# Kernel optimization log

Measured on AMD Instinct MI355X. Metric: run time of the kernel, lower is better.

The kernel has to match this reference:

```python
import math
import jax, jax.numpy as jnp
import numpy as np

LAMDA = 0.5
ALPHA = 0.1
N_NODES = 100000
N_EDGES = 1600000
NFEAT = 512
NHID = 128
NCLASS = 40
NLAYER = 4


def setup_inputs() -> dict:
    key = jax.random.key(0)
    ks = jax.random.split(key, 9)
    x = jax.random.normal(ks[0], (N_NODES, NFEAT), dtype=jnp.float32)
    rows = jnp.sort(jax.random.randint(ks[1], (N_EDGES,), 0, N_NODES, dtype=jnp.int32))
    cols = jax.random.randint(ks[2], (N_EDGES,), 0, N_NODES, dtype=jnp.int32)
    # positive edge weights (stand-in for symmetric-normalized adjacency values)
    vals = jax.random.uniform(ks[3], (N_EDGES,), dtype=jnp.float32) * 0.1
    stdv_hid = 1.0 / math.sqrt(NHID)
    fc1_w = jax.random.normal(ks[4], (NFEAT, NHID), dtype=jnp.float32) * 0.02
    fc1_b = jnp.zeros((NHID,), dtype=jnp.float32)
    conv_w = jax.random.uniform(ks[5], (NLAYER, NHID, NHID), dtype=jnp.float32,
                                minval=-stdv_hid, maxval=stdv_hid)
    fc2_w = jax.random.normal(ks[6], (NHID, NCLASS), dtype=jnp.float32) * 0.02
    fc2_b = jnp.zeros((NCLASS,), dtype=jnp.float32)
    return {"x": x, "rows": rows, "cols": cols, "vals": vals,
            "fc1_w": fc1_w, "fc1_b": fc1_b, "conv_w": conv_w,
            "fc2_w": fc2_w, "fc2_b": fc2_b}


def reference(x, rows, cols, vals, fc1_w, fc1_b, conv_w, fc2_w, fc2_b):
    n = x.shape[0]
    # input projection + relu (dropout is identity in eval mode)
    h = jax.nn.relu(x @ fc1_w + fc1_b)  # [N, nhid]
    h0 = h
    for i in range(conv_w.shape[0]):
        theta = math.log(LAMDA / (i + 1) + 1.0)
        # sparse spmm: hi = A @ h  via gather + segment-sum scatter
        hi = jax.ops.segment_sum(vals[:, None] * h[cols], rows, num_segments=n)
        support = (1.0 - ALPHA) * hi + ALPHA * h0  # initial-residual mix
        h = jax.nn.relu(theta * (support @ conv_w[i]) + (1.0 - theta) * support)
    logits = h @ fc2_w + fc2_b  # [N, nclass]
    return (jax.nn.log_softmax(logits, axis=1), h, jnp.concatenate([h, logits], axis=1))
```

## Files before the change

kernel.cpp:

```cpp
#include <hip/hip_runtime.h>
#include <math.h>

#define N_NODES 100000
#define NFEAT 512
#define NHID 128
#define NCLASS 40

typedef unsigned int uint;
typedef unsigned short ushort;
typedef short bf16x8 __attribute__((ext_vector_type(8)));
typedef float f32x4 __attribute__((ext_vector_type(4)));

__device__ inline ushort bf16s(float a) {
    uint u = __float_as_uint(a);
    return (ushort)((u + 0x7fffu + ((u >> 16) & 1u)) >> 16);
}
__device__ inline uint bf16pack(float a, float b) {
    return (uint)bf16s(a) | ((uint)bf16s(b) << 16);
}
__device__ inline float bf16tof(ushort u) { return __uint_as_float(((uint)u) << 16); }
__device__ inline float bflo(uint u) { return __uint_as_float(u << 16); }
__device__ inline float bfhi(uint u) { return __uint_as_float(u & 0xffff0000u); }

__global__ void prep_weights(const float* __restrict__ fc1_w, const float* __restrict__ conv_w,
                             ushort* __restrict__ wT1, ushort* __restrict__ wTc) {
    int idx = blockIdx.x * 256 + threadIdx.x;
    {   int n = idx >> 9, k = idx & 511;
        wT1[idx] = bf16s(fc1_w[k * NHID + n]); }
    {   int L = idx >> 14, rem = idx & 16383;
        int n = rem >> 7, k = rem & 127;
        wTc[idx] = bf16s(conv_w[L * 16384 + k * NHID + n]); }
}

__global__ void rowptr_kernel(const int* __restrict__ rows, int* __restrict__ rowptr, int nE) {
    int i = blockIdx.x * blockDim.x + threadIdx.x;
    if (i > N_NODES) return;
    int lo = 0, hi = nE;
    while (lo < hi) { int mid = (lo + hi) >> 1; if (rows[mid] < i) lo = mid + 1; else hi = mid; }
    rowptr[i] = lo;
}

__global__ void __launch_bounds__(256) fc1_mfma(const float* __restrict__ x,
                                                const uint* __restrict__ wT1,
                                                const float* __restrict__ bias,
                                                ushort* __restrict__ h0b) {
    __shared__ ushort As[32][72];
    __shared__ ushort Bs[128][72];
    const int tid = threadIdx.x;
    const int lane = tid & 63;
    const int wave = tid >> 6;
    const int wr = wave >> 1, wc = wave & 1;
    const int r0 = blockIdx.x * 32;

    f32x4 acc[4] = {};

    for (int ks = 0; ks < NFEAT; ks += 64) {
        {   int row = tid >> 3, kq = tid & 7;
            const float* xp = x + (size_t)(r0 + row) * NFEAT + ks + kq * 8;
            float4 v0 = *reinterpret_cast<const float4*>(xp);
            float4 v1 = *reinterpret_cast<const float4*>(xp + 4);
            uint4 pk;
            pk.x = bf16pack(v0.x, v0.y); pk.y = bf16pack(v0.z, v0.w);
            pk.z = bf16pack(v1.x, v1.y); pk.w = bf16pack(v1.z, v1.w);
            *reinterpret_cast<uint4*>(&As[row][kq * 8]) = pk;
        }
        #pragma unroll
        for (int p = 0; p < 4; ++p) {
            int idx = tid + p * 256;
            int n = idx >> 3, q = idx & 7;
            uint4 w4 = *reinterpret_cast<const uint4*>(wT1 + n * 256 + (ks >> 1) + q * 4);
            *reinterpret_cast<uint4*>(&Bs[n][q * 8]) = w4;
        }
        __syncthreads();
        #pragma unroll
        for (int ks2 = 0; ks2 < 64; ks2 += 32) {
            bf16x8 a = *reinterpret_cast<const bf16x8*>(&As[wr * 16 + (lane & 15)][ks2 + (lane >> 4) * 8]);
            #pragma unroll
            for (int j = 0; j < 4; ++j) {
                bf16x8 b = *reinterpret_cast<const bf16x8*>(&Bs[wc * 64 + j * 16 + (lane & 15)][ks2 + (lane >> 4) * 8]);
                acc[j] = __builtin_amdgcn_mfma_f32_16x16x32_bf16(a, b, acc[j], 0, 0, 0);
            }
        }
        __syncthreads();
    }

    const int cb = wc * 64 + (lane & 15);
    const int rb = r0 + wr * 16 + ((lane >> 4) << 2);
    #pragma unroll
    for (int j = 0; j < 4; ++j) {
        int col = cb + j * 16;
        float bj = bias[col];
        #pragma unroll
        for (int i = 0; i < 4; ++i) {
            float v = fmaxf(acc[j][i] + bj, 0.f);
            h0b[(size_t)(rb + i) * NHID + col] = bf16s(v);
        }
    }
}

__global__ void __launch_bounds__(256) layer_mfma(const uint* __restrict__ sb,
                                                  const uint* __restrict__ wTc,
                                                  float theta,
                                                  ushort* __restrict__ hb,
                                                  float* __restrict__ fout) {
    __shared__ ushort As[64][136];
    __shared__ ushort Bs[128][136];
    const int tid = threadIdx.x;
    const int lane = tid & 63;
    const int wave = tid >> 6;
    const int wr = wave >> 1, wc = wave & 1;
    const int r0 = blockIdx.x * 64;

    #pragma unroll
    for (int p = 0; p < 4; ++p) {
        int idx = tid + p * 256;
        int row = idx >> 4, kq = idx & 15;
        uint4 v = *reinterpret_cast<const uint4*>(sb + (size_t)(r0 + row) * 64 + kq * 4);
        *reinterpret_cast<uint4*>(&As[row][kq * 8]) = v;
    }
    #pragma unroll
    for (int p = 0; p < 8; ++p) {
        int idx = tid + p * 256;
        int n = idx >> 4, kq = idx & 15;
        uint4 v = *reinterpret_cast<const uint4*>(wTc + n * 64 + kq * 4);
        *reinterpret_cast<uint4*>(&Bs[n][kq * 8]) = v;
    }
    __syncthreads();

    f32x4 acc[2][4] = {};
    #pragma unroll
    for (int ks = 0; ks < NHID; ks += 32) {
        #pragma unroll
        for (int mr = 0; mr < 2; ++mr) {
            bf16x8 a = *reinterpret_cast<const bf16x8*>(&As[wr * 32 + mr * 16 + (lane & 15)][ks + (lane >> 4) * 8]);
            #pragma unroll
            for (int j = 0; j < 4; ++j) {
                bf16x8 b = *reinterpret_cast<const bf16x8*>(&Bs[wc * 64 + j * 16 + (lane & 15)][ks + (lane >> 4) * 8]);
                acc[mr][j] = __builtin_amdgcn_mfma_f32_16x16x32_bf16(a, b, acc[mr][j], 0, 0, 0);
            }
        }
    }

    const float om = 1.f - theta;
    const int cb = wc * 64 + (lane & 15);
    #pragma unroll
    for (int mr = 0; mr < 2; ++mr) {
        const int rloc = wr * 32 + mr * 16 + ((lane >> 4) << 2);
        #pragma unroll
        for (int j = 0; j < 4; ++j) {
            int col = cb + j * 16;
            #pragma unroll
            for (int i = 0; i < 4; ++i) {
                int gr = r0 + rloc + i;
                if (gr < N_NODES) {
                    float s = bf16tof(As[rloc + i][col]);
                    float v = fmaxf(fmaf(theta, acc[mr][j][i], om * s), 0.f);
                    if (fout) fout[(size_t)gr * NHID + col] = v;
                    else      hb[(size_t)gr * NHID + col] = bf16s(v);
                }
            }
        }
    }
}

__global__ void spmm_kernel(const uint4* __restrict__ hb4, const uint4* __restrict__ h0b4,
                            const int* __restrict__ rowptr, const int* __restrict__ cols,
                            const float* __restrict__ vals, uint4* __restrict__ sb4) {
    const int node = blockIdx.x * 4 + (threadIdx.x >> 6);
    const int lane = threadIdx.x & 63;
    const int q = lane >> 4;
    const int l = lane & 15;

    const int e0 = rowptr[node], e1 = rowptr[node + 1];

    float a0 = 0.f, a1 = 0.f, a2 = 0.f, a3 = 0.f;
    float a4 = 0.f, a5 = 0.f, a6 = 0.f, a7 = 0.f;
    for (int base = e0; base < e1; base += 64) {
        int m = e1 - base; if (m > 64) m = 64;
        int c = 0; float v = 0.f;
        if (lane < m) { c = cols[base + lane]; v = vals[base + lane]; }
        const int nt = (m + 3) >> 2;
        #pragma unroll 8
        for (int t = 0; t < nt; ++t) {
            int j = 4 * t + q;
            int jc = (j < m) ? j : 0;
            int   cj = __shfl(c, jc);
            float vj = __shfl(v, jc);
            if (j >= m) vj = 0.f;
            uint4 hv = hb4[(size_t)cj * 16 + l];
            a0 = fmaf(vj, bflo(hv.x), a0);
            a1 = fmaf(vj, bfhi(hv.x), a1);
            a2 = fmaf(vj, bflo(hv.y), a2);
            a3 = fmaf(vj, bfhi(hv.y), a3);
            a4 = fmaf(vj, bflo(hv.z), a4);
            a5 = fmaf(vj, bfhi(hv.z), a5);
            a6 = fmaf(vj, bflo(hv.w), a6);
            a7 = fmaf(vj, bfhi(hv.w), a7);
        }
    }
    a0 += __shfl_xor(a0, 16); a1 += __shfl_xor(a1, 16);
    a2 += __shfl_xor(a2, 16); a3 += __shfl_xor(a3, 16);
    a4 += __shfl_xor(a4, 16); a5 += __shfl_xor(a5, 16);
    a6 += __shfl_xor(a6, 16); a7 += __shfl_xor(a7, 16);
    a0 += __shfl_xor(a0, 32); a1 += __shfl_xor(a1, 32);
    a2 += __shfl_xor(a2, 32); a3 += __shfl_xor(a3, 32);
    a4 += __shfl_xor(a4, 32); a5 += __shfl_xor(a5, 32);
    a6 += __shfl_xor(a6, 32); a7 += __shfl_xor(a7, 32);

    if (q == 0) {
        uint4 h0v = h0b4[(size_t)node * 16 + l];
        uint4 o;
        o.x = bf16pack(0.9f * a0 + 0.1f * bflo(h0v.x), 0.9f * a1 + 0.1f * bfhi(h0v.x));
        o.y = bf16pack(0.9f * a2 + 0.1f * bflo(h0v.y), 0.9f * a3 + 0.1f * bfhi(h0v.y));
        o.z = bf16pack(0.9f * a4 + 0.1f * bflo(h0v.z), 0.9f * a5 + 0.1f * bfhi(h0v.z));
        o.w = bf16pack(0.9f * a6 + 0.1f * bflo(h0v.w), 0.9f * a7 + 0.1f * bfhi(h0v.w));
        sb4[(size_t)node * 16 + l] = o;
    }
}

__global__ void final_kernel(const float* __restrict__ h, const float* __restrict__ w,
                             const float* __restrict__ b, float* __restrict__ out0,
                             float* __restrict__ out2) {
    __shared__ float hs[4][128];
    const int s = threadIdx.x >> 6;
    const int lane = threadIdx.x & 63;
    const int node = blockIdx.x * 4 + s;

    float h_lo = h[node * NHID + lane];
    float h_hi = h[node * NHID + 64 + lane];
    hs[s][lane] = h_lo;
    hs[s][64 + lane] = h_hi;
    __syncthreads();

    float logit = 0.f;
    if (lane < NCLASS) {
        logit = b[lane];
        #pragma unroll 8
        for (int k = 0; k < NHID; ++k)
            logit = fmaf(hs[s][k], w[k * NCLASS + lane], logit);
    }

    float mv = (lane < NCLASS) ? logit : -1e30f;
    #pragma unroll
    for (int m = 32; m; m >>= 1) mv = fmaxf(mv, __shfl_xor(mv, m));
    float ev = (lane < NCLASS) ? __expf(logit - mv) : 0.f;
    float sum = ev;
    #pragma unroll
    for (int m = 32; m; m >>= 1) sum += __shfl_xor(sum, m);
    float lse = mv + __logf(sum);

    if (lane < NCLASS) {
        out0[node * NCLASS + lane] = logit - lse;
        out2[node * 168 + 128 + lane] = logit;
    }
    out2[node * 168 + lane] = h_lo;
    out2[node * 168 + 64 + lane] = h_hi;
}

extern "C" void kernel_launch(void* const* d_in, const int* in_sizes, int n_in,
                              void* d_out, int out_size, void* d_ws, size_t ws_size,
                              hipStream_t stream) {
    const float* x      = (const float*)d_in[0];
    const int*   rows   = (const int*)  d_in[1];
    const int*   cols   = (const int*)  d_in[2];
    const float* vals   = (const float*)d_in[3];
    const float* fc1_w  = (const float*)d_in[4];
    const float* fc1_b  = (const float*)d_in[5];
    const float* conv_w = (const float*)d_in[6];
    const float* fc2_w  = (const float*)d_in[7];
    const float* fc2_b  = (const float*)d_in[8];
    float* out = (float*)d_out;

    const int nE = in_sizes[1];
    const size_t NH = (size_t)N_NODES * NHID;
    const size_t PAD = 64 * NHID;

    char* p = (char*)d_ws;
    int*    rowptr = (int*)p;          p += 400128;
    ushort* h0b    = (ushort*)p;       p += NH * 2;
    ushort* hb     = (ushort*)p;       p += (NH + PAD) * 2;
    ushort* sb     = (ushort*)p;       p += (NH + PAD) * 2;
    ushort* wT1    = (ushort*)p;       p += 65536 * 2;
    ushort* wTc    = (ushort*)p;       p += 65536 * 2;

    float* out0 = out;
    float* out1 = out + (size_t)N_NODES * NCLASS;
    float* out2 = out1 + NH;

    prep_weights<<<256, 256, 0, stream>>>(fc1_w, conv_w, wT1, wTc);
    rowptr_kernel<<<(N_NODES + 1 + 255) / 256, 256, 0, stream>>>(rows, rowptr, nE);
    fc1_mfma<<<N_NODES / 32, 256, 0, stream>>>(x, (const uint*)wT1, fc1_b, h0b);

    for (int i = 0; i < 4; ++i) {
        float theta = logf(0.5f / (float)(i + 1) + 1.0f);
        spmm_kernel<<<N_NODES / 4, 256, 0, stream>>>(
            (const uint4*)(i == 0 ? h0b : hb), (const uint4*)h0b, rowptr, cols, vals, (uint4*)sb);
        layer_mfma<<<(N_NODES + 63) / 64, 256, 0, stream>>>(
            (const uint*)sb, (const uint*)(wTc + (size_t)i * 16384), theta,
            (i < 3) ? hb : nullptr, (i == 3) ? out1 : nullptr);
    }

    final_kernel<<<N_NODES / 4, 256, 0, stream>>>(out1, fc2_w, fc2_b, out0, out2);
}
```

Baseline: 501.2 us.

## Slice feature matrix into 8 column panels so SpMM gathers hit smaller working sets

Hidden activations are now stored as 8 feature slices of 16 columns each (slice-major, padded rows), written by the fc1 and layer GEMM epilogues and read back into LDS by the layer GEMM. The SpMM launches 8 blocks per group of nodes, one per slice, so each random gather touches a 3.2 MB panel instead of the full 25.6 MB matrix, aiming for better L2/MALL hit rates. Edge indices and weights are loaded with nontemporal hints. In exchange, cols/vals are reread 8 times, each gather is only 8 bytes, and more shuffles are needed per edge.

```diff
diff --git a/kernel.cpp b/kernel.cpp
--- a/kernel.cpp
+++ b/kernel.cpp
@@ -2,6 +2,7 @@
 #include <math.h>
 
 #define N_NODES 100000
+#define NPAD    100064
 #define NFEAT 512
 #define NHID 128
 #define NCLASS 40
@@ -21,6 +22,7 @@
 __device__ inline float bf16tof(ushort u) { return __uint_as_float(((uint)u) << 16); }
 __device__ inline float bflo(uint u) { return __uint_as_float(u << 16); }
 __device__ inline float bfhi(uint u) { return __uint_as_float(u & 0xffff0000u); }
+
 
 __global__ void prep_weights(const float* __restrict__ fc1_w, const float* __restrict__ conv_w,
                              ushort* __restrict__ wT1, ushort* __restrict__ wTc) {
@@ -84,21 +86,21 @@
         __syncthreads();
     }
 
-    const int cb = wc * 64 + (lane & 15);
     const int rb = r0 + wr * 16 + ((lane >> 4) << 2);
     #pragma unroll
     for (int j = 0; j < 4; ++j) {
-        int col = cb + j * 16;
+        int col = wc * 64 + j * 16 + (lane & 15);
+        int s = wc * 4 + j;
         float bj = bias[col];
         #pragma unroll
         for (int i = 0; i < 4; ++i) {
             float v = fmaxf(acc[j][i] + bj, 0.f);
-            h0b[(size_t)(rb + i) * NHID + col] = bf16s(v);
-        }
-    }
-}
-
-__global__ void __launch_bounds__(256) layer_mfma(const uint* __restrict__ sb,
+            h0b[((size_t)s * NPAD + rb + i) * 16 + (lane & 15)] = bf16s(v);
+        }
+    }
+}
+
+__global__ void __launch_bounds__(256) layer_mfma(const uint* __restrict__ sbs,
                                                   const uint* __restrict__ wTc,
                                                   float theta,
                                                   ushort* __restrict__ hb,
@@ -114,9 +116,11 @@
     #pragma unroll
     for (int p = 0; p < 4; ++p) {
         int idx = tid + p * 256;
-        int row = idx >> 4, kq = idx & 15;
-        uint4 v = *reinterpret_cast<const uint4*>(sb + (size_t)(r0 + row) * 64 + kq * 4);
-        *reinterpret_cast<uint4*>(&As[row][kq * 8]) = v;
+        int s = idx >> 7;
+        int rem = idx & 127;
+        int row = rem >> 1, half = rem & 1;
+        uint4 v = *reinterpret_cast<const uint4*>(sbs + ((size_t)s * NPAD + r0 + row) * 8 + half * 4);
+        *reinterpret_cast<uint4*>(&As[row][s * 16 + half * 8]) = v;
     }
     #pragma unroll
     for (int p = 0; p < 8; ++p) {
@@ -142,79 +146,75 @@
     }
 
     const float om = 1.f - theta;
-    const int cb = wc * 64 + (lane & 15);
     #pragma unroll
     for (int mr = 0; mr < 2; ++mr) {
         const int rloc = wr * 32 + mr * 16 + ((lane >> 4) << 2);
         #pragma unroll
         for (int j = 0; j < 4; ++j) {
-            int col = cb + j * 16;
+            int col = wc * 64 + j * 16 + (lane & 15);
+            int s = wc * 4 + j;
             #pragma unroll
             for (int i = 0; i < 4; ++i) {
                 int gr = r0 + rloc + i;
                 if (gr < N_NODES) {
-                    float s = bf16tof(As[rloc + i][col]);
-                    float v = fmaxf(fmaf(theta, acc[mr][j][i], om * s), 0.f);
+                    float sv = bf16tof(As[rloc + i][col]);
+                    float v = fmaxf(fmaf(theta, acc[mr][j][i], om * sv), 0.f);
                     if (fout) fout[(size_t)gr * NHID + col] = v;
-                    else      hb[(size_t)gr * NHID + col] = bf16s(v);
+                    else      hb[((size_t)s * NPAD + gr) * 16 + (lane & 15)] = bf16s(v);
                 }
             }
         }
     }
 }
 
-__global__ void spmm_kernel(const uint4* __restrict__ hb4, const uint4* __restrict__ h0b4,
-                            const int* __restrict__ rowptr, const int* __restrict__ cols,
-                            const float* __restrict__ vals, uint4* __restrict__ sb4) {
-    const int node = blockIdx.x * 4 + (threadIdx.x >> 6);
-    const int lane = threadIdx.x & 63;
-    const int q = lane >> 4;
-    const int l = lane & 15;
+__global__ void __launch_bounds__(256) spmm_kernel(const uint2* __restrict__ hbs,
+                                                   const uint2* __restrict__ h0bs,
+                                                   const int* __restrict__ rowptr,
+                                                   const int* __restrict__ cols,
+                                                   const float* __restrict__ vals,
+                                                   uint2* __restrict__ sbs) {
+    const int slice = blockIdx.x & 7;
+    const int node  = (blockIdx.x >> 3) * 4 + (threadIdx.x >> 6);
+    const int lane  = threadIdx.x & 63;
+    const int slot  = lane >> 2;
+    const int fl    = lane & 3;
 
     const int e0 = rowptr[node], e1 = rowptr[node + 1];
+    const uint2* hrow = hbs + (size_t)slice * NPAD * 4;
 
     float a0 = 0.f, a1 = 0.f, a2 = 0.f, a3 = 0.f;
-    float a4 = 0.f, a5 = 0.f, a6 = 0.f, a7 = 0.f;
-    for (int base = e0; base < e1; base += 64) {
-        int m = e1 - base; if (m > 64) m = 64;
+    #pragma unroll 2
+    for (int base = e0; base < e1; base += 16) {
+        int m = e1 - base; if (m > 16) m = 16;
         int c = 0; float v = 0.f;
-        if (lane < m) { c = cols[base + lane]; v = vals[base + lane]; }
-        const int nt = (m + 3) >> 2;
-        #pragma unroll 8
-        for (int t = 0; t < nt; ++t) {
-            int j = 4 * t + q;
-            int jc = (j < m) ? j : 0;
-            int   cj = __shfl(c, jc);
-            float vj = __shfl(v, jc);
-            if (j >= m) vj = 0.f;
-            uint4 hv = hb4[(size_t)cj * 16 + l];
-            a0 = fmaf(vj, bflo(hv.x), a0);
-            a1 = fmaf(vj, bfhi(hv.x), a1);
-            a2 = fmaf(vj, bflo(hv.y), a2);
-            a3 = fmaf(vj, bfhi(hv.y), a3);
-            a4 = fmaf(vj, bflo(hv.z), a4);
-            a5 = fmaf(vj, bfhi(hv.z), a5);
-            a6 = fmaf(vj, bflo(hv.w), a6);
-            a7 = fmaf(vj, bfhi(hv.w), a7);
-        }
-    }
-    a0 += __shfl_xor(a0, 16); a1 += __shfl_xor(a1, 16);
-    a2 += __shfl_xor(a2, 16); a3 += __shfl_xor(a3, 16);
-    a4 += __shfl_xor(a4, 16); a5 += __shfl_xor(a5, 16);
-    a6 += __shfl_xor(a6, 16); a7 += __shfl_xor(a7, 16);
-    a0 += __shfl_xor(a0, 32); a1 += __shfl_xor(a1, 32);
-    a2 += __shfl_xor(a2, 32); a3 += __shfl_xor(a3, 32);
-    a4 += __shfl_xor(a4, 32); a5 += __shfl_xor(a5, 32);
-    a6 += __shfl_xor(a6, 32); a7 += __shfl_xor(a7, 32);
-
-    if (q == 0) {
-        uint4 h0v = h0b4[(size_t)node * 16 + l];
-        uint4 o;
-        o.x = bf16pack(0.9f * a0 + 0.1f * bflo(h0v.x), 0.9f * a1 + 0.1f * bfhi(h0v.x));
-        o.y = bf16pack(0.9f * a2 + 0.1f * bflo(h0v.y), 0.9f * a3 + 0.1f * bfhi(h0v.y));
-        o.z = bf16pack(0.9f * a4 + 0.1f * bflo(h0v.z), 0.9f * a5 + 0.1f * bfhi(h0v.z));
-        o.w = bf16pack(0.9f * a6 + 0.1f * bflo(h0v.w), 0.9f * a7 + 0.1f * bfhi(h0v.w));
-        sb4[(size_t)node * 16 + l] = o;
+        if (lane < m) {
+            c = __builtin_nontemporal_load(cols + base + lane);
+            v = __builtin_nontemporal_load(vals + base + lane);
+        }
+        int   cj = __shfl(c, slot);
+        float vj = __shfl(v, slot);
+        if (slot >= m) vj = 0.f;
+        uint2 hv = hrow[(size_t)cj * 4 + fl];
+        a0 = fmaf(vj, bflo(hv.x), a0);
+        a1 = fmaf(vj, bfhi(hv.x), a1);
+        a2 = fmaf(vj, bflo(hv.y), a2);
+        a3 = fmaf(vj, bfhi(hv.y), a3);
+    }
+    #pragma unroll
+    for (int d = 4; d <= 32; d <<= 1) {
+        a0 += __shfl_xor(a0, d);
+        a1 += __shfl_xor(a1, d);
+        a2 += __shfl_xor(a2, d);
+        a3 += __shfl_xor(a3, d);
+    }
+
+    if (slot == 0) {
+        size_t o = ((size_t)slice * NPAD + node) * 4 + fl;
+        uint2 h0v = h0bs[o];
+        uint2 w;
+        w.x = bf16pack(0.9f * a0 + 0.1f * bflo(h0v.x), 0.9f * a1 + 0.1f * bfhi(h0v.x));
+        w.y = bf16pack(0.9f * a2 + 0.1f * bflo(h0v.y), 0.9f * a3 + 0.1f * bfhi(h0v.y));
+        sbs[o] = w;
     }
 }
 
@@ -272,20 +272,19 @@
     float* out = (float*)d_out;
 
     const int nE = in_sizes[1];
-    const size_t NH = (size_t)N_NODES * NHID;
-    const size_t PAD = 64 * NHID;
+    const size_t SLICED = (size_t)8 * NPAD * 16;
 
     char* p = (char*)d_ws;
     int*    rowptr = (int*)p;          p += 400128;
-    ushort* h0b    = (ushort*)p;       p += NH * 2;
-    ushort* hb     = (ushort*)p;       p += (NH + PAD) * 2;
-    ushort* sb     = (ushort*)p;       p += (NH + PAD) * 2;
+    ushort* h0b    = (ushort*)p;       p += SLICED * 2;
+    ushort* hb     = (ushort*)p;       p += SLICED * 2;
+    ushort* sb     = (ushort*)p;       p += SLICED * 2;
     ushort* wT1    = (ushort*)p;       p += 65536 * 2;
     ushort* wTc    = (ushort*)p;       p += 65536 * 2;
 
     float* out0 = out;
     float* out1 = out + (size_t)N_NODES * NCLASS;
-    float* out2 = out1 + NH;
+    float* out2 = out1 + (size_t)N_NODES * NHID;
 
     prep_weights<<<256, 256, 0, stream>>>(fc1_w, conv_w, wT1, wTc);
     rowptr_kernel<<<(N_NODES + 1 + 255) / 256, 256, 0, stream>>>(rows, rowptr, nE);
@@ -293,8 +292,8 @@
 
     for (int i = 0; i < 4; ++i) {
         float theta = logf(0.5f / (float)(i + 1) + 1.0f);
-        spmm_kernel<<<N_NODES / 4, 256, 0, stream>>>(
-            (const uint4*)(i == 0 ? h0b : hb), (const uint4*)h0b, rowptr, cols, vals, (uint4*)sb);
+        spmm_kernel<<<(N_NODES / 4) * 8, 256, 0, stream>>>(
+            (const uint2*)(i == 0 ? h0b : hb), (const uint2*)h0b, rowptr, cols, vals, (uint2*)sb);
         layer_mfma<<<(N_NODES + 63) / 64, 256, 0, stream>>>(
             (const uint*)sb, (const uint*)(wTc + (size_t)i * 16384), theta,
             (i < 3) ? hb : nullptr, (i == 3) ? out1 : nullptr);
```

Result: slower. 1.334 ms (+166.2%).

## Fuse SpMM gather with per-layer MFMA GEMM into a single kernel

Applied to the files above, without the earlier changes.

Merges the sparse aggregation and the dense layer GEMM into one kernel per layer. Each 64-row block computes the support rows into LDS and then runs the MFMA transform directly, so the bf16 support buffer no longer makes a round trip through global memory and one launch per layer is removed. Ping-pong buffers replace in-place hb reuse. The weight tile is split into two K halves to shrink LDS and allow 4 blocks per CU. The tradeoff is far fewer waves per node (each wave serially processes 16 rows instead of one block per 4 nodes), which may reduce gather latency hiding and adds load imbalance within blocks.

```diff
diff --git a/kernel.cpp b/kernel.cpp
--- a/kernel.cpp
+++ b/kernel.cpp
@@ -98,57 +98,127 @@
     }
 }
 
-__global__ void __launch_bounds__(256) layer_mfma(const uint* __restrict__ sb,
-                                                  const uint* __restrict__ wTc,
-                                                  float theta,
-                                                  ushort* __restrict__ hb,
-                                                  float* __restrict__ fout) {
+__global__ void __launch_bounds__(256, 4) spmm_layer(
+        const uint4* __restrict__ hsrc,
+        const uint4* __restrict__ h0b4,
+        const int* __restrict__ rowptr,
+        const int* __restrict__ cols,
+        const float* __restrict__ vals,
+        const uint* __restrict__ wTc,
+        float theta,
+        ushort* __restrict__ hb,
+        float* __restrict__ fout) {
     __shared__ ushort As[64][136];
-    __shared__ ushort Bs[128][136];
-    const int tid = threadIdx.x;
+    __shared__ ushort Bs[128][72];
+    const int tid  = threadIdx.x;
     const int lane = tid & 63;
     const int wave = tid >> 6;
-    const int wr = wave >> 1, wc = wave & 1;
-    const int r0 = blockIdx.x * 64;
+    const int r0   = blockIdx.x * 64;
+    const int q = lane >> 4;
+    const int l = lane & 15;
 
     #pragma unroll
     for (int p = 0; p < 4; ++p) {
         int idx = tid + p * 256;
-        int row = idx >> 4, kq = idx & 15;
-        uint4 v = *reinterpret_cast<const uint4*>(sb + (size_t)(r0 + row) * 64 + kq * 4);
-        *reinterpret_cast<uint4*>(&As[row][kq * 8]) = v;
-    }
-    #pragma unroll
-    for (int p = 0; p < 8; ++p) {
-        int idx = tid + p * 256;
-        int n = idx >> 4, kq = idx & 15;
+        int n = idx >> 3, kq = idx & 7;
         uint4 v = *reinterpret_cast<const uint4*>(wTc + n * 64 + kq * 4);
         *reinterpret_cast<uint4*>(&Bs[n][kq * 8]) = v;
     }
+
+    for (int n0 = 0; n0 < 16; ++n0) {
+        const int row  = wave * 16 + n0;
+        const int node = r0 + row;
+        int e0 = 0, e1 = 0;
+        if (node < N_NODES) { e0 = rowptr[node]; e1 = rowptr[node + 1]; }
+
+        float a0 = 0.f, a1 = 0.f, a2 = 0.f, a3 = 0.f;
+        float a4 = 0.f, a5 = 0.f, a6 = 0.f, a7 = 0.f;
+        for (int base = e0; base < e1; base += 64) {
+            int m = e1 - base; if (m > 64) m = 64;
+            int c = 0; float v = 0.f;
+            if (lane < m) { c = cols[base + lane]; v = vals[base + lane]; }
+            const int nt = (m + 3) >> 2;
+            #pragma unroll 8
+            for (int t = 0; t < nt; ++t) {
+                int j = 4 * t + q;
+                int jc = (j < m) ? j : 0;
+                int   cj = __shfl(c, jc);
+                float vj = __shfl(v, jc);
+                if (j >= m) vj = 0.f;
+                uint4 hv = hsrc[(size_t)cj * 16 + l];
+                a0 = fmaf(vj, bflo(hv.x), a0);
+                a1 = fmaf(vj, bfhi(hv.x), a1);
+                a2 = fmaf(vj, bflo(hv.y), a2);
+                a3 = fmaf(vj, bfhi(hv.y), a3);
+                a4 = fmaf(vj, bflo(hv.z), a4);
+                a5 = fmaf(vj, bfhi(hv.z), a5);
+                a6 = fmaf(vj, bflo(hv.w), a6);
+                a7 = fmaf(vj, bfhi(hv.w), a7);
+            }
+        }
+        a0 += __shfl_xor(a0, 16); a1 += __shfl_xor(a1, 16);
+        a2 += __shfl_xor(a2, 16); a3 += __shfl_xor(a3, 16);
+        a4 += __shfl_xor(a4, 16); a5 += __shfl_xor(a5, 16);
+        a6 += __shfl_xor(a6, 16); a7 += __shfl_xor(a7, 16);
+        a0 += __shfl_xor(a0, 32); a1 += __shfl_xor(a1, 32);
+        a2 += __shfl_xor(a2, 32); a3 += __shfl_xor(a3, 32);
+        a4 += __shfl_xor(a4, 32); a5 += __shfl_xor(a5, 32);
+        a6 += __shfl_xor(a6, 32); a7 += __shfl_xor(a7, 32);
+
+        if (q == 0) {
+            uint4 o;
+            if (node < N_NODES) {
+                uint4 h0v = h0b4[(size_t)node * 16 + l];
+                o.x = bf16pack(0.9f * a0 + 0.1f * bflo(h0v.x), 0.9f * a1 + 0.1f * bfhi(h0v.x));
+                o.y = bf16pack(0.9f * a2 + 0.1f * bflo(h0v.y), 0.9f * a3 + 0.1f * bfhi(h0v.y));
+                o.z = bf16pack(0.9f * a4 + 0.1f * bflo(h0v.z), 0.9f * a5 + 0.1f * bfhi(h0v.z));
+                o.w = bf16pack(0.9f * a6 + 0.1f * bflo(h0v.w), 0.9f * a7 + 0.1f * bfhi(h0v.w));
+            } else {
+                o.x = o.y = o.z = o.w = 0u;
+            }
+            *reinterpret_cast<uint4*>(&As[row][l * 8]) = o;
+        }
+    }
     __syncthreads();
 
+    const int wr = wave >> 1, wc = wave & 1;
     f32x4 acc[2][4] = {};
     #pragma unroll
-    for (int ks = 0; ks < NHID; ks += 32) {
-        #pragma unroll
-        for (int mr = 0; mr < 2; ++mr) {
-            bf16x8 a = *reinterpret_cast<const bf16x8*>(&As[wr * 32 + mr * 16 + (lane & 15)][ks + (lane >> 4) * 8]);
+    for (int halfk = 0; halfk < 2; ++halfk) {
+        if (halfk) {
+            __syncthreads();
             #pragma unroll
-            for (int j = 0; j < 4; ++j) {
-                bf16x8 b = *reinterpret_cast<const bf16x8*>(&Bs[wc * 64 + j * 16 + (lane & 15)][ks + (lane >> 4) * 8]);
-                acc[mr][j] = __builtin_amdgcn_mfma_f32_16x16x32_bf16(a, b, acc[mr][j], 0, 0, 0);
+            for (int p = 0; p < 4; ++p) {
+                int idx = tid + p * 256;
+                int n = idx >> 3, kq = idx & 7;
+                uint4 v = *reinterpret_cast<const uint4*>(wTc + n * 64 + 32 + kq * 4);
+                *reinterpret_cast<uint4*>(&Bs[n][kq * 8]) = v;
+            }
+            __syncthreads();
+        }
+        #pragma unroll
+        for (int ks2 = 0; ks2 < 64; ks2 += 32) {
+            #pragma unroll
+            for (int mr = 0; mr < 2; ++mr) {
+                bf16x8 a = *reinterpret_cast<const bf16x8*>(
+                    &As[wr * 32 + mr * 16 + (lane & 15)][halfk * 64 + ks2 + (lane >> 4) * 8]);
+                #pragma unroll
+                for (int j = 0; j < 4; ++j) {
+                    bf16x8 b = *reinterpret_cast<const bf16x8*>(
+                        &Bs[wc * 64 + j * 16 + (lane & 15)][ks2 + (lane >> 4) * 8]);
+                    acc[mr][j] = __builtin_amdgcn_mfma_f32_16x16x32_bf16(a, b, acc[mr][j], 0, 0, 0);
+                }
             }
         }
     }
 
     const float om = 1.f - theta;
-    const int cb = wc * 64 + (lane & 15);
     #pragma unroll
     for (int mr = 0; mr < 2; ++mr) {
         const int rloc = wr * 32 + mr * 16 + ((lane >> 4) << 2);
         #pragma unroll
         for (int j = 0; j < 4; ++j) {
-            int col = cb + j * 16;
+            int col = wc * 64 + j * 16 + (lane & 15);
             #pragma unroll
             for (int i = 0; i < 4; ++i) {
                 int gr = r0 + rloc + i;
@@ -160,61 +230,6 @@
                 }
             }
         }
-    }
-}
-
-__global__ void spmm_kernel(const uint4* __restrict__ hb4, const uint4* __restrict__ h0b4,
-                            const int* __restrict__ rowptr, const int* __restrict__ cols,
-                            const float* __restrict__ vals, uint4* __restrict__ sb4) {
-    const int node = blockIdx.x * 4 + (threadIdx.x >> 6);
-    const int lane = threadIdx.x & 63;
-    const int q = lane >> 4;
-    const int l = lane & 15;
-
-    const int e0 = rowptr[node], e1 = rowptr[node + 1];
-
-    float a0 = 0.f, a1 = 0.f, a2 = 0.f, a3 = 0.f;
-    float a4 = 0.f, a5 = 0.f, a6 = 0.f, a7 = 0.f;
-    for (int base = e0; base < e1; base += 64) {
-        int m = e1 - base; if (m > 64) m = 64;
-        int c = 0; float v = 0.f;
-        if (lane < m) { c = cols[base + lane]; v = vals[base + lane]; }
-        const int nt = (m + 3) >> 2;
-        #pragma unroll 8
-        for (int t = 0; t < nt; ++t) {
-            int j = 4 * t + q;
-            int jc = (j < m) ? j : 0;
-            int   cj = __shfl(c, jc);
-            float vj = __shfl(v, jc);
-            if (j >= m) vj = 0.f;
-            uint4 hv = hb4[(size_t)cj * 16 + l];
-            a0 = fmaf(vj, bflo(hv.x), a0);
-            a1 = fmaf(vj, bfhi(hv.x), a1);
-            a2 = fmaf(vj, bflo(hv.y), a2);
-            a3 = fmaf(vj, bfhi(hv.y), a3);
-            a4 = fmaf(vj, bflo(hv.z), a4);
-            a5 = fmaf(vj, bfhi(hv.z), a5);
-            a6 = fmaf(vj, bflo(hv.w), a6);
-            a7 = fmaf(vj, bfhi(hv.w), a7);
-        }
-    }
-    a0 += __shfl_xor(a0, 16); a1 += __shfl_xor(a1, 16);
-    a2 += __shfl_xor(a2, 16); a3 += __shfl_xor(a3, 16);
-    a4 += __shfl_xor(a4, 16); a5 += __shfl_xor(a5, 16);
-    a6 += __shfl_xor(a6, 16); a7 += __shfl_xor(a7, 16);
-    a0 += __shfl_xor(a0, 32); a1 += __shfl_xor(a1, 32);
-    a2 += __shfl_xor(a2, 32); a3 += __shfl_xor(a3, 32);
-    a4 += __shfl_xor(a4, 32); a5 += __shfl_xor(a5, 32);
-    a6 += __shfl_xor(a6, 32); a7 += __shfl_xor(a7, 32);
-
-    if (q == 0) {
-        uint4 h0v = h0b4[(size_t)node * 16 + l];
-        uint4 o;
-        o.x = bf16pack(0.9f * a0 + 0.1f * bflo(h0v.x), 0.9f * a1 + 0.1f * bfhi(h0v.x));
-        o.y = bf16pack(0.9f * a2 + 0.1f * bflo(h0v.y), 0.9f * a3 + 0.1f * bfhi(h0v.y));
-        o.z = bf16pack(0.9f * a4 + 0.1f * bflo(h0v.z), 0.9f * a5 + 0.1f * bfhi(h0v.z));
-        o.w = bf16pack(0.9f * a6 + 0.1f * bflo(h0v.w), 0.9f * a7 + 0.1f * bfhi(h0v.w));
-        sb4[(size_t)node * 16 + l] = o;
     }
 }
 
@@ -273,13 +288,12 @@
 
     const int nE = in_sizes[1];
     const size_t NH = (size_t)N_NODES * NHID;
-    const size_t PAD = 64 * NHID;
 
     char* p = (char*)d_ws;
     int*    rowptr = (int*)p;          p += 400128;
     ushort* h0b    = (ushort*)p;       p += NH * 2;
-    ushort* hb     = (ushort*)p;       p += (NH + PAD) * 2;
-    ushort* sb     = (ushort*)p;       p += (NH + PAD) * 2;
+    ushort* bufA   = (ushort*)p;       p += NH * 2;
+    ushort* bufB   = (ushort*)p;       p += NH * 2;
     ushort* wT1    = (ushort*)p;       p += 65536 * 2;
     ushort* wTc    = (ushort*)p;       p += 65536 * 2;
 
@@ -291,13 +305,16 @@
     rowptr_kernel<<<(N_NODES + 1 + 255) / 256, 256, 0, stream>>>(rows, rowptr, nE);
     fc1_mfma<<<N_NODES / 32, 256, 0, stream>>>(x, (const uint*)wT1, fc1_b, h0b);
 
+    const int nblk = (N_NODES + 63) / 64;
+    const ushort* src = h0b;
+    ushort* dsts[4] = { bufA, bufB, bufA, nullptr };
     for (int i = 0; i < 4; ++i) {
         float theta = logf(0.5f / (float)(i + 1) + 1.0f);
-        spmm_kernel<<<N_NODES / 4, 256, 0, stream>>>(
-            (const uint4*)(i == 0 ? h0b : hb), (const uint4*)h0b, rowptr, cols, vals, (uint4*)sb);
-        layer_mfma<<<(N_NODES + 63) / 64, 256, 0, stream>>>(
-            (const uint*)sb, (const uint*)(wTc + (size_t)i * 16384), theta,
-            (i < 3) ? hb : nullptr, (i == 3) ? out1 : nullptr);
+        spmm_layer<<<nblk, 256, 0, stream>>>(
+            (const uint4*)src, (const uint4*)h0b, rowptr, cols, vals,
+            (const uint*)(wTc + (size_t)i * 16384), theta,
+            dsts[i], (i == 3) ? out1 : nullptr);
+        src = dsts[i];
     }
 
     final_kernel<<<N_NODES / 4, 256, 0, stream>>>(out1, fc2_w, fc2_b, out0, out2);
```

After: 640.2 us. 27.7% more time.
